# Optimization experiments

Measured on AMD Instinct MI355X. Metric: run time of the kernel, lower is better.

Reference implementation:

```python
import jax, jax.numpy as jnp
import numpy as np

D_MODEL = 1024
NUM_HEADS = 16
HEAD_DIM = D_MODEL // NUM_HEADS  # d_k = d_v = 64


def setup_inputs() -> dict:
    key = jax.random.key(0)
    ks = jax.random.split(key, 11)
    B, S = 2, 2048
    s = 1.0 / np.sqrt(D_MODEL)
    inp = {
        "query": jax.random.normal(ks[0], (B, S, D_MODEL), jnp.float32),
        "key": jax.random.normal(ks[1], (B, S, D_MODEL), jnp.float32),
        "value": jax.random.normal(ks[2], (B, S, D_MODEL), jnp.float32),
        "Wq": jax.random.normal(ks[3], (D_MODEL, D_MODEL), jnp.float32) * s,
        "bq": jax.random.normal(ks[4], (D_MODEL,), jnp.float32) * s,
        "Wk": jax.random.normal(ks[5], (D_MODEL, D_MODEL), jnp.float32) * s,
        "bk": jax.random.normal(ks[6], (D_MODEL,), jnp.float32) * s,
        "Wv": jax.random.normal(ks[7], (D_MODEL, D_MODEL), jnp.float32) * s,
        "bv": jax.random.normal(ks[8], (D_MODEL,), jnp.float32) * s,
        "Wo": jax.random.normal(ks[9], (D_MODEL, D_MODEL), jnp.float32) * s,
        "bo": jax.random.normal(ks[10], (D_MODEL,), jnp.float32) * s,
    }
    return inp


def reference(query, key, value, Wq, bq, Wk, bk, Wv, bv, Wo, bo):
    B, Sq, _ = query.shape
    # Linear projections (torch Linear: x @ W.T + b), split into heads
    def proj(x, W, b):
        y = x @ W.T + b  # [B, S, d_model]
        return y.reshape(B, -1, NUM_HEADS, HEAD_DIM).transpose(0, 2, 1, 3)  # [B, H, S, d]

    Q = proj(query, Wq, bq)
    K = proj(key, Wk, bk)
    V = proj(value, Wv, bv)

    scale = 1.0 / jnp.sqrt(jnp.asarray(HEAD_DIM, Q.dtype))
    scores = jnp.einsum("bhqd,bhkd->bhqk", Q, K) * scale  # [B, H, Sq, Sk]
    attn = jax.nn.softmax(scores, axis=-1)
    out = jnp.einsum("bhqk,bhkd->bhqd", attn, V)  # [B, H, Sq, d]
    out = out.transpose(0, 2, 1, 3).reshape(B, Sq, NUM_HEADS * HEAD_DIM)
    return out @ Wo.T + bo
```

## Files before the change

kernel.cpp:

```cpp
#include <hip/hip_runtime.h>
#include <hip/hip_bf16.h>

#define D_MODEL 1024
#define NHEADS  16
#define HDIM    64
#define BATCH   2
#define SEQ     2048
#define MTOT    (BATCH*SEQ)

typedef __attribute__((ext_vector_type(8))) short bf16x8;
typedef __attribute__((ext_vector_type(4))) float f32x4;

__device__ __forceinline__ void async_load16(const void* g, void* l) {
    __builtin_amdgcn_global_load_lds(
        (const __attribute__((address_space(1))) void*)g,
        (__attribute__((address_space(3))) void*)l, 16, 0, 0);
}

__device__ __forceinline__ short f2b(float x) {
    unsigned u = __builtin_bit_cast(unsigned, x) + 0x8000u;
    return (short)(u >> 16);
}
__device__ __forceinline__ unsigned pack2(float lo, float hi) {
    unsigned ulo = __builtin_bit_cast(unsigned, lo) + 0x8000u;
    unsigned uhi = __builtin_bit_cast(unsigned, hi) + 0x8000u;
    return __builtin_amdgcn_perm(uhi, ulo, 0x07060302u);
}

__global__ void cvt_all(const float* __restrict__ s0, const float* __restrict__ s1,
                        const float* __restrict__ s2, const float* __restrict__ s3,
                        const float* __restrict__ s4, const float* __restrict__ s5,
                        const float* __restrict__ s6,
                        short* __restrict__ d0, short* __restrict__ d1,
                        short* __restrict__ d2, short* __restrict__ d3,
                        short* __restrict__ d4, short* __restrict__ d5,
                        short* __restrict__ d6) {
    int bx = blockIdx.x;
    const float* src; short* dst; int blk;
    if (bx < 6144) {
        int t = bx >> 11; blk = bx & 2047;
        src = t == 0 ? s0 : (t == 1 ? s1 : s2);
        dst = t == 0 ? d0 : (t == 1 ? d1 : d2);
    } else {
        int t = (bx - 6144) >> 9; blk = (bx - 6144) & 511;
        src = t == 0 ? s3 : (t == 1 ? s4 : (t == 2 ? s5 : s6));
        dst = t == 0 ? d3 : (t == 1 ? d4 : (t == 2 ? d5 : d6));
    }
    int i = (blk * 256 + threadIdx.x) * 8;
    const float4* s4p = (const float4*)(src + i);
    float4 a = s4p[0], b = s4p[1];
    unsigned u0 = pack2(a.x, a.y), u1 = pack2(a.z, a.w);
    unsigned u2 = pack2(b.x, b.y), u3 = pack2(b.z, b.w);
    uint4 o; o.x = u0; o.y = u1; o.z = u2; o.w = u3;
    *(uint4*)(dst + i) = o;
}

__device__ __forceinline__ void gemm_core(const short* __restrict__ A,
                                          const short* __restrict__ Bt,
                                          int K, int m0, int n0,
                                          f32x4 (&acc)[4][4]) {
    __shared__ short As[128 * 32];
    __shared__ short Bs[128 * 32];
    const int lane = threadIdx.x & 63;
    const int wid  = threadIdx.x >> 6;
    const int wm   = (wid >> 1) * 64;
    const int wn   = (wid & 1) * 64;
    const int q    = lane & 15;
    const int quad = lane >> 4;
    const int lr   = lane >> 2;
    const int swzs = (lr + (lr >> 2)) & 3;
    const int cA   = (((lane & 3) ^ swzs)) * 8;
    const int kg   = (quad ^ ((q + (q >> 2)) & 3)) * 8;

#pragma unroll
    for (int mi = 0; mi < 4; mi++)
#pragma unroll
        for (int ni = 0; ni < 4; ni++)
            acc[mi][ni] = f32x4{0.f, 0.f, 0.f, 0.f};

    for (int k0 = 0; k0 < K; k0 += 32) {
#pragma unroll
        for (int c = 0; c < 2; ++c) {
            int chunk = wid * 2 + c;
            const short* ga = A  + (size_t)(m0 + chunk * 16 + lr) * K + k0 + cA;
            async_load16(ga, (char*)As + chunk * 1024);
            const short* gb = Bt + (size_t)(n0 + chunk * 16 + lr) * K + k0 + cA;
            async_load16(gb, (char*)Bs + chunk * 1024);
        }
        __syncthreads();
        bf16x8 af[4], bfr[4];
#pragma unroll
        for (int mi = 0; mi < 4; mi++)
            af[mi] = *(const bf16x8*)&As[(wm + mi * 16 + q) * 32 + kg];
#pragma unroll
        for (int ni = 0; ni < 4; ni++)
            bfr[ni] = *(const bf16x8*)&Bs[(wn + ni * 16 + q) * 32 + kg];
#pragma unroll
        for (int mi = 0; mi < 4; mi++)
#pragma unroll
            for (int ni = 0; ni < 4; ni++)
                acc[mi][ni] = __builtin_amdgcn_mfma_f32_16x16x32_bf16(
                    af[mi], bfr[ni], acc[mi][ni], 0, 0, 0);
        __syncthreads();
    }
}

#define QSCALE (0.125f * 1.44269504f)
__global__ __launch_bounds__(256) void proj_qkv(
    const short* __restrict__ xq, const short* __restrict__ xk, const short* __restrict__ xv,
    const short* __restrict__ wq, const short* __restrict__ wk, const short* __restrict__ wv,
    const float* __restrict__ bq, const float* __restrict__ bk, const float* __restrict__ bv,
    short* __restrict__ Qo, short* __restrict__ Ko, short* __restrict__ Vo) {
    const int z = blockIdx.z;
    const short* A    = z == 0 ? xq : (z == 1 ? xk : xv);
    const short* Bt   = z == 0 ? wq : (z == 1 ? wk : wv);
    const float* bias = z == 0 ? bq : (z == 1 ? bk : bv);
    short*       Out  = z == 0 ? Qo : (z == 1 ? Ko : Vo);
    const float scale = (z == 0) ? QSCALE : 1.0f;

    const int m0 = blockIdx.y * 128, n0 = blockIdx.x * 128;
    f32x4 acc[4][4];
    gemm_core(A, Bt, D_MODEL, m0, n0, acc);

    const int lane = threadIdx.x & 63;
    const int wid  = threadIdx.x >> 6;
    const int q = lane & 15, quad = lane >> 4;
    const int wm = (wid >> 1) * 64, wn = (wid & 1) * 64;
#pragma unroll
    for (int mi = 0; mi < 4; mi++)
#pragma unroll
        for (int ni = 0; ni < 4; ni++)
#pragma unroll
            for (int r = 0; r < 4; r++) {
                int m = m0 + wm + mi * 16 + quad * 4 + r;
                int n = n0 + wn + ni * 16 + q;
                float v = (acc[mi][ni][r] + bias[n]) * scale;
                int b = m >> 11, s = m & (SEQ - 1);
                int h = n >> 6, d = n & 63;
                Out[((size_t)(b * NHEADS + h) * SEQ + s) * HDIM + d] = f2b(v);
            }
}

__global__ __launch_bounds__(256) void gemm_out(
    const short* __restrict__ O, const short* __restrict__ wo,
    const float* __restrict__ bo, float* __restrict__ out) {
    const int m0 = blockIdx.y * 128, n0 = blockIdx.x * 128;
    f32x4 acc[4][4];
    gemm_core(O, wo, D_MODEL, m0, n0, acc);

    const int lane = threadIdx.x & 63;
    const int wid  = threadIdx.x >> 6;
    const int wm = (wid >> 1) * 64, wn = (wid & 1) * 64;
#pragma unroll
    for (int mi = 0; mi < 4; mi++)
#pragma unroll
        for (int ni = 0; ni < 4; ni++)
#pragma unroll
            for (int r = 0; r < 4; r++) {
                int m = m0 + wm + mi * 16 + (lane >> 4) * 4 + r;
                int n = n0 + wn + ni * 16 + (lane & 15);
                out[(size_t)m * D_MODEL + n] = acc[mi][ni][r] + bo[n];
            }
}

__global__ __launch_bounds__(256) void transpose_v(const short* __restrict__ Vp,
                                                   short* __restrict__ Vt) {
    const int bh = blockIdx.y, ts = blockIdx.x;
    __shared__ short T[64][72];
    const int tid = threadIdx.x;
    const int r = tid >> 2, c = (tid & 3) * 16;
    const bf16x8* g = (const bf16x8*)(Vp + ((size_t)bh * SEQ + ts * 64 + r) * HDIM + c);
    *(bf16x8*)&T[r][c]     = g[0];
    *(bf16x8*)&T[r][c + 8] = g[1];
    __syncthreads();
    bf16x8 o0, o1;
#pragma unroll
    for (int j = 0; j < 8; j++) o0[j] = T[c + j][r];
#pragma unroll
    for (int j = 0; j < 8; j++) o1[j] = T[c + 8 + j][r];
    short* dst = Vt + ((size_t)bh * HDIM + r) * SEQ + ts * 64 + c;
    *(bf16x8*)dst = o0;
    *(bf16x8*)(dst + 8) = o1;
}

#define C2 24.0f
__global__ __launch_bounds__(256, 2) void attn(
    const short* __restrict__ Q, const short* __restrict__ K,
    const short* __restrict__ Vt, short* __restrict__ O) {
    const int n = blockIdx.x;
    const int bh = ((n >> 7) << 3) | (n & 7);
    const int qb = (n >> 3) & 15;
    const int b = bh >> 4, h = bh & 15;
    const int lane = threadIdx.x & 63;
    const int w = threadIdx.x >> 6;
    const int wq = w & 1, wk = w >> 1;
    const int q0 = qb * 128 + wq * 64;
    const int q = lane & 15, quad = lane >> 4;
    const short* Qb  = Q + (size_t)bh * SEQ * HDIM;
    const short* Kb  = K + (size_t)bh * SEQ * HDIM;
    const short* Vtb = Vt + (size_t)bh * HDIM * SEQ;

    bf16x8 qf[4][2];
#pragma unroll
    for (int g = 0; g < 4; ++g)
#pragma unroll
        for (int c = 0; c < 2; ++c)
            qf[g][c] = *(const bf16x8*)(Qb + (size_t)(q0 + g * 16 + q) * HDIM +
                                        c * 32 + quad * 8);

    float lpart[4] = {0.f, 0.f, 0.f, 0.f};
    f32x4 oacc[4][4];
#pragma unroll
    for (int g = 0; g < 4; ++g)
#pragma unroll
        for (int dt = 0; dt < 4; dt++) oacc[g][dt] = f32x4{0.f, 0.f, 0.f, 0.f};

    const int s0l = ((quad & 1) << 5) | q;
    const int s1l = s0l + 16;

    for (int kt = wk; kt < SEQ / 64; kt += 2) {
        const short* Kt = Kb + (size_t)kt * 64 * HDIM;
        bf16x8 kf[2][4], vf[2][4];
#pragma unroll
        for (int t = 0; t < 4; t++)
#pragma unroll
            for (int c = 0; c < 2; ++c)
                kf[c][t] = *(const bf16x8*)(Kt + (size_t)(t * 16 + q) * HDIM +
                                            c * 32 + quad * 8);
#pragma unroll
        for (int dt = 0; dt < 4; dt++)
#pragma unroll
            for (int c = 0; c < 2; ++c)
                vf[c][dt] = *(const bf16x8*)(Vtb + (size_t)(dt * 16 + q) * SEQ +
                                             kt * 64 + c * 32 + quad * 8);

#pragma unroll
        for (int g = 0; g < 4; ++g) {
            f32x4 st[4];
#pragma unroll
            for (int t = 0; t < 4; t++) {
                f32x4 s = f32x4{0.f, 0.f, 0.f, 0.f};
                s = __builtin_amdgcn_mfma_f32_16x16x32_bf16(kf[0][t], qf[g][0], s, 0, 0, 0);
                s = __builtin_amdgcn_mfma_f32_16x16x32_bf16(kf[1][t], qf[g][1], s, 0, 0, 0);
                st[t] = s;
            }
            float lp = lpart[g];
#pragma unroll
            for (int t = 0; t < 4; t++)
#pragma unroll
                for (int r = 0; r < 4; r++) {
                    float p = __builtin_amdgcn_exp2f(st[t][r] - C2);
                    st[t][r] = p;
                    lp += p;
                }
            lpart[g] = lp;
            unsigned pk[4][2];
#pragma unroll
            for (int t = 0; t < 4; t++) {
                pk[t][0] = pack2(st[t][0], st[t][1]);
                pk[t][1] = pack2(st[t][2], st[t][3]);
            }
            bf16x8 pb[2];
#pragma unroll
            for (int c = 0; c < 2; ++c) {
                unsigned lo0 = __shfl(pk[2 * c][0], s0l);
                unsigned lo1 = __shfl(pk[2 * c][1], s0l);
                unsigned lo2 = __shfl(pk[2 * c][0], s1l);
                unsigned lo3 = __shfl(pk[2 * c][1], s1l);
                unsigned hi0 = __shfl(pk[2 * c + 1][0], s0l);
                unsigned hi1 = __shfl(pk[2 * c + 1][1], s0l);
                unsigned hi2 = __shfl(pk[2 * c + 1][0], s1l);
                unsigned hi3 = __shfl(pk[2 * c + 1][1], s1l);
                uint4 u;
                u.x = quad < 2 ? lo0 : hi0;
                u.y = quad < 2 ? lo1 : hi1;
                u.z = quad < 2 ? lo2 : hi2;
                u.w = quad < 2 ? lo3 : hi3;
                pb[c] = __builtin_bit_cast(bf16x8, u);
            }
#pragma unroll
            for (int dt = 0; dt < 4; dt++) {
                oacc[g][dt] = __builtin_amdgcn_mfma_f32_16x16x32_bf16(vf[0][dt], pb[0],
                                                                     oacc[g][dt], 0, 0, 0);
                oacc[g][dt] = __builtin_amdgcn_mfma_f32_16x16x32_bf16(vf[1][dt], pb[1],
                                                                     oacc[g][dt], 0, 0, 0);
            }
        }
    }

    __shared__ f32x4 redO[4][4][64];
    __shared__ float redL[4][64];
#pragma unroll
    for (int g = 0; g < 4; ++g) {
        __syncthreads();
        redL[w][lane] = lpart[g];
#pragma unroll
        for (int dt = 0; dt < 4; dt++) redO[w][dt][lane] = oacc[g][dt];
        __syncthreads();
        float lt = 0.f;
#pragma unroll
        for (int wk2 = 0; wk2 < 2; ++wk2)
#pragma unroll
            for (int qd = 0; qd < 4; ++qd) lt += redL[wq + wk2 * 2][qd * 16 + q];
        const float inv = 1.f / lt;
        const int qg = q0 + g * 16 + q;
        short* orow = O + ((size_t)(b * SEQ + qg)) * D_MODEL + h * HDIM;
#pragma unroll
        for (int dd = 0; dd < 2; ++dd) {
            const int dt = wk * 2 + dd;
            f32x4 o = redO[wq][dt][lane];
            f32x4 t2 = redO[wq + 2][dt][lane];
#pragma unroll
            for (int r = 0; r < 4; r++) o[r] += t2[r];
            short4 s4;
            s4.x = f2b(o[0] * inv);
            s4.y = f2b(o[1] * inv);
            s4.z = f2b(o[2] * inv);
            s4.w = f2b(o[3] * inv);
            *(short4*)(orow + dt * 16 + quad * 4) = s4;
        }
    }
}

extern "C" void kernel_launch(void* const* d_in, const int* in_sizes, int n_in,
                              void* d_out, int out_size, void* d_ws, size_t ws_size,
                              hipStream_t stream) {
    (void)in_sizes; (void)n_in; (void)out_size; (void)ws_size;
    const float* q_in = (const float*)d_in[0];
    const float* k_in = (const float*)d_in[1];
    const float* v_in = (const float*)d_in[2];
    const float* Wq   = (const float*)d_in[3];
    const float* bq   = (const float*)d_in[4];
    const float* Wk   = (const float*)d_in[5];
    const float* bk   = (const float*)d_in[6];
    const float* Wv   = (const float*)d_in[7];
    const float* bv   = (const float*)d_in[8];
    const float* Wo   = (const float*)d_in[9];
    const float* bo   = (const float*)d_in[10];
    float* out = (float*)d_out;

    constexpr size_t MB = 1ull << 20;
    char* ws = (char*)d_ws;
    short* xq  = (short*)(ws + 0 * MB);
    short* xk  = (short*)(ws + 8 * MB);
    short* xv  = (short*)(ws + 16 * MB);
    short* wqb = (short*)(ws + 24 * MB);
    short* wkb = (short*)(ws + 26 * MB);
    short* wvb = (short*)(ws + 28 * MB);
    short* wob = (short*)(ws + 30 * MB);
    short* Qp  = (short*)(ws + 32 * MB);
    short* Kp  = (short*)(ws + 40 * MB);
    short* Vp  = (short*)(ws + 48 * MB);
    short* Op  = (short*)(ws + 56 * MB);
    short* VtG = (short*)(ws + 0 * MB);

    cvt_all<<<8192, 256, 0, stream>>>(q_in, k_in, v_in, Wq, Wk, Wv, Wo,
                                      xq, xk, xv, wqb, wkb, wvb, wob);
    proj_qkv<<<dim3(8, 32, 3), 256, 0, stream>>>(xq, xk, xv, wqb, wkb, wvb,
                                                 bq, bk, bv, Qp, Kp, Vp);
    transpose_v<<<dim3(SEQ / 64, BATCH * NHEADS), 256, 0, stream>>>(Vp, VtG);
    attn<<<512, 256, 0, stream>>>(Qp, Kp, VtG, Op);
    gemm_out<<<dim3(8, 32), 256, 0, stream>>>(Op, wob, bo, out);
}
```

Baseline: 251.3 us.

## Deepen GEMM K-tile to 64, halve attention query tile, prefetch K fragments

The shared GEMM core now stages 64-wide K slices per iteration with an XOR swizzle across 8 column groups. This halves the number of barriers per GEMM at the cost of twice the LDS. The attention kernel processes 32 query rows per wave instead of 64, doubling the grid to 1024 blocks for more parallelism and lower register pressure. It also software-prefetches the next K tile into registers while computing the current one. The prefetch reads one tile past the end on the last iterations, which is out-of-bounds for the final head.

```diff
diff --git a/kernel.cpp b/kernel.cpp
--- a/kernel.cpp
+++ b/kernel.cpp
@@ -49,9 +49,9 @@
     int i = (blk * 256 + threadIdx.x) * 8;
     const float4* s4p = (const float4*)(src + i);
     float4 a = s4p[0], b = s4p[1];
-    unsigned u0 = pack2(a.x, a.y), u1 = pack2(a.z, a.w);
-    unsigned u2 = pack2(b.x, b.y), u3 = pack2(b.z, b.w);
-    uint4 o; o.x = u0; o.y = u1; o.z = u2; o.w = u3;
+    uint4 o;
+    o.x = pack2(a.x, a.y); o.y = pack2(a.z, a.w);
+    o.z = pack2(b.x, b.y); o.w = pack2(b.z, b.w);
     *(uint4*)(dst + i) = o;
 }
 
@@ -59,18 +59,17 @@
                                           const short* __restrict__ Bt,
                                           int K, int m0, int n0,
                                           f32x4 (&acc)[4][4]) {
-    __shared__ short As[128 * 32];
-    __shared__ short Bs[128 * 32];
+    __shared__ short As[128 * 64];
+    __shared__ short Bs[128 * 64];
     const int lane = threadIdx.x & 63;
     const int wid  = threadIdx.x >> 6;
     const int wm   = (wid >> 1) * 64;
     const int wn   = (wid & 1) * 64;
     const int q    = lane & 15;
     const int quad = lane >> 4;
-    const int lr   = lane >> 2;
-    const int swzs = (lr + (lr >> 2)) & 3;
-    const int cA   = (((lane & 3) ^ swzs)) * 8;
-    const int kg   = (quad ^ ((q + (q >> 2)) & 3)) * 8;
+    const int lr8  = lane >> 3;
+    const int colA = ((lane & 7) ^ lr8) * 8;
+    const int pgq  = q & 7;
 
 #pragma unroll
     for (int mi = 0; mi < 4; mi++)
@@ -78,29 +77,34 @@
         for (int ni = 0; ni < 4; ni++)
             acc[mi][ni] = f32x4{0.f, 0.f, 0.f, 0.f};
 
-    for (int k0 = 0; k0 < K; k0 += 32) {
-#pragma unroll
-        for (int c = 0; c < 2; ++c) {
-            int chunk = wid * 2 + c;
-            const short* ga = A  + (size_t)(m0 + chunk * 16 + lr) * K + k0 + cA;
-            async_load16(ga, (char*)As + chunk * 1024);
-            const short* gb = Bt + (size_t)(n0 + chunk * 16 + lr) * K + k0 + cA;
-            async_load16(gb, (char*)Bs + chunk * 1024);
+    for (int k0 = 0; k0 < K; k0 += 64) {
+#pragma unroll
+        for (int i = 0; i < 4; ++i) {
+            const int rowbase = wid * 32 + i * 8;
+            async_load16(A  + (size_t)(m0 + rowbase + lr8) * K + k0 + colA,
+                         (char*)As + rowbase * 128);
+            async_load16(Bt + (size_t)(n0 + rowbase + lr8) * K + k0 + colA,
+                         (char*)Bs + rowbase * 128);
         }
         __syncthreads();
-        bf16x8 af[4], bfr[4];
-#pragma unroll
-        for (int mi = 0; mi < 4; mi++)
-            af[mi] = *(const bf16x8*)&As[(wm + mi * 16 + q) * 32 + kg];
-#pragma unroll
-        for (int ni = 0; ni < 4; ni++)
-            bfr[ni] = *(const bf16x8*)&Bs[(wn + ni * 16 + q) * 32 + kg];
-#pragma unroll
-        for (int mi = 0; mi < 4; mi++)
+#pragma unroll
+        for (int ki = 0; ki < 2; ++ki) {
+            bf16x8 af[4], bfr[4];
+#pragma unroll
+            for (int mi = 0; mi < 4; mi++)
+                af[mi] = *(const bf16x8*)&As[(wm + mi * 16 + q) * 64 +
+                                             ((ki * 4 + quad) ^ pgq) * 8];
 #pragma unroll
             for (int ni = 0; ni < 4; ni++)
-                acc[mi][ni] = __builtin_amdgcn_mfma_f32_16x16x32_bf16(
-                    af[mi], bfr[ni], acc[mi][ni], 0, 0, 0);
+                bfr[ni] = *(const bf16x8*)&Bs[(wn + ni * 16 + q) * 64 +
+                                              ((ki * 4 + quad) ^ pgq) * 8];
+#pragma unroll
+            for (int mi = 0; mi < 4; mi++)
+#pragma unroll
+                for (int ni = 0; ni < 4; ni++)
+                    acc[mi][ni] = __builtin_amdgcn_mfma_f32_16x16x32_bf16(
+                        af[mi], bfr[ni], acc[mi][ni], 0, 0, 0);
+        }
         __syncthreads();
     }
 }
@@ -188,54 +192,67 @@
     const short* __restrict__ Q, const short* __restrict__ K,
     const short* __restrict__ Vt, short* __restrict__ O) {
     const int n = blockIdx.x;
-    const int bh = ((n >> 7) << 3) | (n & 7);
-    const int qb = (n >> 3) & 15;
+    const int bh = ((n >> 8) << 3) | (n & 7);
+    const int qt = (n >> 3) & 31;
     const int b = bh >> 4, h = bh & 15;
     const int lane = threadIdx.x & 63;
     const int w = threadIdx.x >> 6;
     const int wq = w & 1, wk = w >> 1;
-    const int q0 = qb * 128 + wq * 64;
+    const int q0 = qt * 64 + wq * 32;
     const int q = lane & 15, quad = lane >> 4;
     const short* Qb  = Q + (size_t)bh * SEQ * HDIM;
     const short* Kb  = K + (size_t)bh * SEQ * HDIM;
     const short* Vtb = Vt + (size_t)bh * HDIM * SEQ;
 
-    bf16x8 qf[4][2];
-#pragma unroll
-    for (int g = 0; g < 4; ++g)
+    bf16x8 qf[2][2];
+#pragma unroll
+    for (int g = 0; g < 2; ++g)
 #pragma unroll
         for (int c = 0; c < 2; ++c)
             qf[g][c] = *(const bf16x8*)(Qb + (size_t)(q0 + g * 16 + q) * HDIM +
                                         c * 32 + quad * 8);
 
-    float lpart[4] = {0.f, 0.f, 0.f, 0.f};
-    f32x4 oacc[4][4];
-#pragma unroll
-    for (int g = 0; g < 4; ++g)
+    float lpart[2] = {0.f, 0.f};
+    f32x4 oacc[2][4];
+#pragma unroll
+    for (int g = 0; g < 2; ++g)
 #pragma unroll
         for (int dt = 0; dt < 4; dt++) oacc[g][dt] = f32x4{0.f, 0.f, 0.f, 0.f};
 
     const int s0l = ((quad & 1) << 5) | q;
     const int s1l = s0l + 16;
 
-    for (int kt = wk; kt < SEQ / 64; kt += 2) {
-        const short* Kt = Kb + (size_t)kt * 64 * HDIM;
-        bf16x8 kf[2][4], vf[2][4];
+    bf16x8 kf[2][4];
+    {
+        const short* Kt = Kb + (size_t)wk * 64 * HDIM;
 #pragma unroll
         for (int t = 0; t < 4; t++)
 #pragma unroll
             for (int c = 0; c < 2; ++c)
                 kf[c][t] = *(const bf16x8*)(Kt + (size_t)(t * 16 + q) * HDIM +
                                             c * 32 + quad * 8);
+    }
+
+    for (int kt = wk; kt < SEQ / 64; kt += 2) {
+        bf16x8 vf[2][4], kn[2][4];
 #pragma unroll
         for (int dt = 0; dt < 4; dt++)
 #pragma unroll
             for (int c = 0; c < 2; ++c)
                 vf[c][dt] = *(const bf16x8*)(Vtb + (size_t)(dt * 16 + q) * SEQ +
                                              kt * 64 + c * 32 + quad * 8);
-
-#pragma unroll
-        for (int g = 0; g < 4; ++g) {
+        {
+            const short* Kn = Kb + (size_t)(kt + 2) * 64 * HDIM;
+#pragma unroll
+            for (int t = 0; t < 4; t++)
+#pragma unroll
+                for (int c = 0; c < 2; ++c)
+                    kn[c][t] = *(const bf16x8*)(Kn + (size_t)(t * 16 + q) * HDIM +
+                                                c * 32 + quad * 8);
+        }
+
+#pragma unroll
+        for (int g = 0; g < 2; ++g) {
             f32x4 st[4];
 #pragma unroll
             for (int t = 0; t < 4; t++) {
@@ -286,12 +303,16 @@
                                                                      oacc[g][dt], 0, 0, 0);
             }
         }
+#pragma unroll
+        for (int t = 0; t < 4; t++)
+#pragma unroll
+            for (int c = 0; c < 2; ++c) kf[c][t] = kn[c][t];
     }
 
     __shared__ f32x4 redO[4][4][64];
     __shared__ float redL[4][64];
 #pragma unroll
-    for (int g = 0; g < 4; ++g) {
+    for (int g = 0; g < 2; ++g) {
         __syncthreads();
         redL[w][lane] = lpart[g];
 #pragma unroll
@@ -301,7 +322,7 @@
 #pragma unroll
         for (int wk2 = 0; wk2 < 2; ++wk2)
 #pragma unroll
-            for (int qd = 0; qd < 4; ++qd) lt += redL[wq + wk2 * 2][qd * 16 + q];
+            for (int qd = 0; qd < 4; ++qd) lt += redL[wk2 * 2 + wq][qd * 16 + q];
         const float inv = 1.f / lt;
         const int qg = q0 + g * 16 + q;
         short* orow = O + ((size_t)(b * SEQ + qg)) * D_MODEL + h * HDIM;
@@ -359,6 +380,6 @@
     proj_qkv<<<dim3(8, 32, 3), 256, 0, stream>>>(xq, xk, xv, wqb, wkb, wvb,
                                                  bq, bk, bv, Qp, Kp, Vp);
     transpose_v<<<dim3(SEQ / 64, BATCH * NHEADS), 256, 0, stream>>>(Vp, VtG);
-    attn<<<512, 256, 0, stream>>>(Qp, Kp, VtG, Op);
+    attn<<<1024, 256, 0, stream>>>(Qp, Kp, VtG, Op);
     gemm_out<<<dim3(8, 32), 256, 0, stream>>>(Op, wob, bo, out);
 }
```

Result: slower. 305.3 us (+21.5%).
